# Optimization experiments

Measured on AMD Instinct MI355X. Metric: run time of the kernel, lower is better.

## Reference

```python
import jax, jax.numpy as jnp
import numpy as np

EPS = 1e-5


def _linear(x, w, b):
    # torch Linear: y = x @ w.T + b, w shape [out, in]
    return x @ w.T + b


def _batchnorm(x, gamma, beta):
    # training-mode BatchNorm1d: per-feature batch stats, biased variance
    m = jnp.mean(x, axis=0)
    v = jnp.var(x, axis=0)
    return (x - m) * jax.lax.rsqrt(v + EPS) * gamma + beta


def _noise_like(key, x):
    # mimics: mean = x.mean().item(); std = x.std().item() * U(1,2);
    # noise ~ N(mean, std) of x.shape, detached.
    ku, kn = jax.random.split(key)
    m = jax.lax.stop_gradient(jnp.mean(x))
    s = jax.lax.stop_gradient(jnp.std(x, ddof=1))
    u = jax.random.uniform(ku, (), dtype=x.dtype, minval=1.0, maxval=2.0)
    return m + s * u * jax.random.normal(kn, x.shape, dtype=x.dtype)


def setup_inputs() -> dict:
    key = jax.random.key(0)
    ks = jax.random.split(key, 12)
    B = 65536
    x = jax.random.normal(ks[0], (B, 784), dtype=jnp.float32)

    def lin_init(kw, kb, fan_in, fan_out):
        bound = 1.0 / np.sqrt(fan_in)
        w = jax.random.uniform(kw, (fan_out, fan_in), minval=-bound, maxval=bound, dtype=jnp.float32)
        b = jax.random.uniform(kb, (fan_out,), minval=-bound, maxval=bound, dtype=jnp.float32)
        return w, b

    w1, b1 = lin_init(ks[1], ks[2], 784, 48)
    w2, b2 = lin_init(ks[3], ks[4], 48, 24)
    w3, b3 = lin_init(ks[5], ks[6], 24, 10)
    return {
        "x": x,
        "w1": w1, "b1": b1,
        "gamma1": jnp.ones((48,), jnp.float32), "beta1": jnp.zeros((48,), jnp.float32),
        "w2": w2, "b2": b2,
        "gamma2": jnp.ones((24,), jnp.float32), "beta2": jnp.zeros((24,), jnp.float32),
        "w3": w3, "b3": b3,
    }


def reference(x, w1, b1, gamma1, beta1, w2, b2, gamma2, beta2, w3, b3):
    k1 = jax.random.key(1234)
    k2 = jax.random.key(5678)
    h = _batchnorm(_linear(x, w1, b1), gamma1, beta1)
    h = h + _noise_like(k1, h)
    h = jax.nn.relu(h)
    h = _batchnorm(_linear(h, w2, b2), gamma2, beta2)
    h = h + _noise_like(k2, h)
    h = jax.nn.relu(h)
    return _linear(h, w3, b3)
```

## Files before the change

### kernel.cpp

```cpp
#include <hip/hip_runtime.h>
#include <cstdint>
#include <cstring>


constexpr int MROWS = 65536;
constexpr int KDIM  = 784;
constexpr int KPAD  = 800;
constexpr int F1 = 48, F2 = 24, F3 = 10;

using frag_ab = __attribute__((ext_vector_type(8))) short;
using frag_cd = __attribute__((ext_vector_type(4))) float;

union UB { uint4 u; frag_ab f; };

__device__ __forceinline__ uint32_t rotl32(uint32_t v, int r) {
  return (v << r) | (v >> (32 - r));
}

__device__ __forceinline__ uint32_t tf_mix(uint32_t k0, uint32_t k1, uint32_t ctr) {
  uint32_t ks2 = k0 ^ k1 ^ 0x1BD11BDAu;
  uint32_t x0 = k0;
  uint32_t x1 = ctr + k1;
#define TFR(r) { x0 += x1; x1 = rotl32(x1, r); x1 ^= x0; }
  TFR(13) TFR(15) TFR(26) TFR(6)
  x0 += k1;  x1 += ks2 + 1u;
  TFR(17) TFR(29) TFR(16) TFR(24)
  x0 += ks2; x1 += k0 + 2u;
  TFR(13) TFR(15) TFR(26) TFR(6)
  x0 += k0;  x1 += k1 + 3u;
  TFR(17) TFR(29) TFR(16) TFR(24)
  x0 += k1;  x1 += ks2 + 4u;
  TFR(13) TFR(15) TFR(26) TFR(6)
  x0 += ks2; x1 += k0 + 5u;
#undef TFR
  return x0 ^ x1;
}

__device__ __forceinline__ float erfinv_f32(float x) {
  float t = fmaxf(1.0f - x * x, 1.0e-30f);
  float w = -__logf(t);
  float p;
  if (w < 5.0f) {
    w = w - 2.5f;
    p = 2.81022636e-08f;
    p = fmaf(p, w, 3.43273939e-07f);
    p = fmaf(p, w, -3.5233877e-06f);
    p = fmaf(p, w, -4.39150654e-06f);
    p = fmaf(p, w, 0.00021858087f);
    p = fmaf(p, w, -0.00125372503f);
    p = fmaf(p, w, -0.00417768164f);
    p = fmaf(p, w, 0.246640727f);
    p = fmaf(p, w, 1.50140941f);
  } else {
    w = sqrtf(w) - 3.0f;
    p = -0.000200214257f;
    p = fmaf(p, w, 0.000100950558f);
    p = fmaf(p, w, 0.00134934322f);
    p = fmaf(p, w, -0.00367342844f);
    p = fmaf(p, w, 0.00573950773f);
    p = fmaf(p, w, -0.0076224613f);
    p = fmaf(p, w, 0.00943887047f);
    p = fmaf(p, w, 1.00167406f);
    p = fmaf(p, w, 2.83297682f);
  }
  return p * x;
}

__device__ __forceinline__ float noise_normal(uint32_t k0, uint32_t k1, uint32_t ctr) {
  uint32_t bits = tf_mix(k0, k1, ctr);
  float f = __uint_as_float((bits >> 9) | 0x3f800000u) - 1.0f;
  const float lo = -0.99999994f;
  float u = fmaxf(lo, f * 2.0f + lo);
  return 1.41421356f * erfinv_f32(u);
}

__device__ __forceinline__ uint32_t pkbf(float a, float b) {
  uint32_t ua = __float_as_uint(a); ua += 0x7fffu + ((ua >> 16) & 1u);
  uint32_t ub = __float_as_uint(b); ub += 0x7fffu + ((ub >> 16) & 1u);
  return (ua >> 16) | (ub & 0xffff0000u);
}

__device__ __forceinline__ uint32_t cvtpk(float a, float b) {
  uint32_t r;
  asm("v_cvt_pk_bf16_f32 %0, %1, %2" : "=v"(r) : "v"(a), "v"(b));
  return r;
}

__global__ void k_prep(const float* __restrict__ w1, ushort* __restrict__ wb1,
                       float* __restrict__ st) {
  int i = blockIdx.x * 256 + threadIdx.x;
  if (i < 2048) st[i] = 0.f;
  if (i >= F1 * KPAD) return;
  int n = i / KPAD, k = i - n * KPAD;
  float v = (k < KDIM) ? w1[n * KDIM + k] : 0.f;
  uint32_t u = __float_as_uint(v);
  u += 0x7fffu + ((u >> 16) & 1u);
  wb1[i] = (ushort)(u >> 16);
}

__global__ __launch_bounds__(256, 4) void k_gemm1(
    const float* __restrict__ x, const ushort* __restrict__ wb1,
    const float* __restrict__ b1, float* __restrict__ h1,
    float* __restrict__ fsum, float* __restrict__ fssq) {
  __shared__ float reds[4][48], redq[4][48];

  const int t = threadIdx.x;
  const int w = t >> 6;
  const int l = t & 63;
  const int lane16 = l & 15;
  const int quad = l >> 4;
  const int rowbase = blockIdx.x * 64;
  const int myrow = rowbase + w * 16 + lane16;

  frag_cd acc[3];
#pragma unroll
  for (int ct = 0; ct < 3; ++ct)
#pragma unroll
    for (int r = 0; r < 4; ++r) acc[ct][r] = 0.f;

  const float* ap = x + (size_t)myrow * KDIM + quad * 8;
  const ushort* bp0 = wb1 + (size_t)(0 * 16 + lane16) * KPAD + quad * 8;
  const ushort* bp1 = wb1 + (size_t)(1 * 16 + lane16) * KPAD + quad * 8;
  const ushort* bp2 = wb1 + (size_t)(2 * 16 + lane16) * KPAD + quad * 8;

  float4 ca0 = *(const float4*)(ap);
  float4 ca1 = *(const float4*)(ap + 4);
  uint4 cb0 = *(const uint4*)(bp0);
  uint4 cb1 = *(const uint4*)(bp1);
  uint4 cb2 = *(const uint4*)(bp2);

  for (int s = 0; s < 25; ++s) {
    float4 na0 = make_float4(0.f, 0.f, 0.f, 0.f);
    float4 na1 = na0;
    uint4 nb0 = make_uint4(0, 0, 0, 0), nb1 = nb0, nb2 = nb0;
    if (s < 24) {
      const int ko = (s + 1) * 32;
      if (ko + quad * 8 + 8 <= KDIM) {
        na0 = *(const float4*)(ap + ko);
        na1 = *(const float4*)(ap + ko + 4);
      }
      nb0 = *(const uint4*)(bp0 + ko);
      nb1 = *(const uint4*)(bp1 + ko);
      nb2 = *(const uint4*)(bp2 + ko);
    }
    UB a;
    a.u.x = cvtpk(ca0.x, ca0.y);
    a.u.y = cvtpk(ca0.z, ca0.w);
    a.u.z = cvtpk(ca1.x, ca1.y);
    a.u.w = cvtpk(ca1.z, ca1.w);
    UB b;
    b.u = cb0; acc[0] = __builtin_amdgcn_mfma_f32_16x16x32_bf16(a.f, b.f, acc[0], 0, 0, 0);
    b.u = cb1; acc[1] = __builtin_amdgcn_mfma_f32_16x16x32_bf16(a.f, b.f, acc[1], 0, 0, 0);
    b.u = cb2; acc[2] = __builtin_amdgcn_mfma_f32_16x16x32_bf16(a.f, b.f, acc[2], 0, 0, 0);
    ca0 = na0; ca1 = na1; cb0 = nb0; cb1 = nb1; cb2 = nb2;
  }

  float bias[3];
#pragma unroll
  for (int ct = 0; ct < 3; ++ct) bias[ct] = b1[ct * 16 + lane16];
  float psum[3] = {0.f, 0.f, 0.f}, pssq[3] = {0.f, 0.f, 0.f};
#pragma unroll
  for (int r = 0; r < 4; ++r) {
    const int grow = rowbase + w * 16 + quad * 4 + r;
#pragma unroll
    for (int ct = 0; ct < 3; ++ct) {
      float v = acc[ct][r] + bias[ct];
      h1[(size_t)grow * F1 + ct * 16 + lane16] = v;
      psum[ct] += v;
      pssq[ct] += v * v;
    }
  }
#pragma unroll
  for (int ct = 0; ct < 3; ++ct) {
    psum[ct] += __shfl_xor(psum[ct], 16, 64);
    psum[ct] += __shfl_xor(psum[ct], 32, 64);
    pssq[ct] += __shfl_xor(pssq[ct], 16, 64);
    pssq[ct] += __shfl_xor(pssq[ct], 32, 64);
  }
  if (quad == 0) {
#pragma unroll
    for (int ct = 0; ct < 3; ++ct) {
      reds[w][ct * 16 + lane16] = psum[ct];
      redq[w][ct * 16 + lane16] = pssq[ct];
    }
  }
  __syncthreads();
  if (t < F1) {
    float s = reds[0][t] + reds[1][t] + reds[2][t] + reds[3][t];
    float q = redq[0][t] + redq[1][t] + redq[2][t] + redq[3][t];
    const int rep = blockIdx.x & 7;
    atomicAdd(&fsum[rep * 48 + t], s);
    atomicAdd(&fssq[rep * 48 + t], q);
  }
}

__global__ __launch_bounds__(256) void k_layer2(
    const float* __restrict__ h1, const float* __restrict__ w2,
    const float* __restrict__ b2, const float* __restrict__ gamma1,
    const float* __restrict__ beta1, const float* __restrict__ fsum,
    const float* __restrict__ fssq, float u1,
    float* __restrict__ h2, float* __restrict__ fsum2, float* __restrict__ fssq2,
    uint32_t kna, uint32_t knb) {
  __shared__ float a1s[64][49];
  __shared__ float w2s[48][25];
  __shared__ float h2s[64][25];
  __shared__ float bnp[4][48];
  __shared__ float scal[2];

  const int t = threadIdx.x;
  const int rowbase = blockIdx.x * 64;

  float cm = 0.f, cs = 0.f;
  if (t < F1) {
    float s0 = 0.f, q0 = 0.f;
#pragma unroll
    for (int rp = 0; rp < 8; ++rp) { s0 += fsum[rp * 48 + t]; q0 += fssq[rp * 48 + t]; }
    float m = s0 * (1.f / 65536.f);
    float v = q0 * (1.f / 65536.f) - m * m;
    float r = rsqrtf(v + 1e-5f);
    float g = gamma1[t], b = beta1[t];
    bnp[0][t] = m; bnp[1][t] = r; bnp[2][t] = g; bnp[3][t] = b;
    cm = b;
    cs = g * g * r * r * v + b * b;
  }
  if (t < 64) {
#pragma unroll
    for (int off = 32; off > 0; off >>= 1) {
      cm += __shfl_down(cm, off, 64);
      cs += __shfl_down(cs, off, 64);
    }
    if (t == 0) {
      float m = cm / (float)F1;
      float SS = 65536.f * cs;
      float Ntot = 65536.f * (float)F1;
      float s2 = (SS - Ntot * m * m) / (Ntot - 1.f);
      scal[0] = m;
      scal[1] = sqrtf(s2) * u1;
    }
  }
  for (int e = t; e < F2 * 48; e += 256) {
    int c = e / 48, k = e - c * 48;
    w2s[k][c] = w2[e];
  }
  __syncthreads();
  const float m1 = scal[0], su1 = scal[1];

  const int rr = t >> 2;
  const int cc0 = (t & 3) * 12;
  const int grow = rowbase + rr;
  const float* hrow = h1 + (size_t)grow * F1 + cc0;
#pragma unroll
  for (int jj = 0; jj < 12; jj += 4) {
    float4 hv = *(const float4*)(hrow + jj);
    float vv[4] = {hv.x, hv.y, hv.z, hv.w};
#pragma unroll
    for (int q = 0; q < 4; ++q) {
      int c = cc0 + jj + q;
      float bn = (vv[q] - bnp[0][c]) * bnp[1][c] * bnp[2][c] + bnp[3][c];
      uint32_t ctr = (uint32_t)grow * 48u + (uint32_t)c;
      float nz = noise_normal(kna, knb, ctr);
      float val = bn + fmaf(su1, nz, m1);
      a1s[rr][c] = fmaxf(val, 0.f);
    }
  }
  __syncthreads();

  const int rr2 = t & 63;
  const int c0 = (t >> 6) * 6;
  float acc[6] = {0.f, 0.f, 0.f, 0.f, 0.f, 0.f};
#pragma unroll
  for (int k = 0; k < 48; ++k) {
    float a = a1s[rr2][k];
#pragma unroll
    for (int j = 0; j < 6; ++j)
      acc[j] = fmaf(a, w2s[k][c0 + j], acc[j]);
  }
#pragma unroll
  for (int j = 0; j < 6; ++j)
    h2s[rr2][c0 + j] = acc[j] + b2[c0 + j];
  __syncthreads();

  for (int e = t; e < 64 * F2; e += 256) {
    int r2 = e / 24, c2 = e - r2 * 24;
    h2[(size_t)rowbase * F2 + e] = h2s[r2][c2];
  }
  if (t < F2) {
    float s = 0.f, q = 0.f;
    for (int r2 = 0; r2 < 64; ++r2) {
      float v = h2s[r2][t];
      s += v; q += v * v;
    }
    const int rep = blockIdx.x & 7;
    atomicAdd(&fsum2[rep * 24 + t], s);
    atomicAdd(&fssq2[rep * 24 + t], q);
  }
}

__global__ __launch_bounds__(256) void k_layer3(
    const float* __restrict__ h2, const float* __restrict__ w3,
    const float* __restrict__ b3, const float* __restrict__ gamma2,
    const float* __restrict__ beta2, const float* __restrict__ fsum2,
    const float* __restrict__ fssq2, float u2,
    float* __restrict__ out, uint32_t kna, uint32_t knb) {
  __shared__ float a2s[64][25];
  __shared__ float w3s[24][10];
  __shared__ float bnp[4][24];
  __shared__ float scal[2];

  const int t = threadIdx.x;
  const int rowbase = blockIdx.x * 64;

  float cm = 0.f, cs = 0.f;
  if (t < F2) {
    float s0 = 0.f, q0 = 0.f;
#pragma unroll
    for (int rp = 0; rp < 8; ++rp) { s0 += fsum2[rp * 24 + t]; q0 += fssq2[rp * 24 + t]; }
    float m = s0 * (1.f / 65536.f);
    float v = q0 * (1.f / 65536.f) - m * m;
    float r = rsqrtf(v + 1e-5f);
    float g = gamma2[t], b = beta2[t];
    bnp[0][t] = m; bnp[1][t] = r; bnp[2][t] = g; bnp[3][t] = b;
    cm = b;
    cs = g * g * r * r * v + b * b;
  }
  if (t < 64) {
#pragma unroll
    for (int off = 32; off > 0; off >>= 1) {
      cm += __shfl_down(cm, off, 64);
      cs += __shfl_down(cs, off, 64);
    }
    if (t == 0) {
      float m = cm / (float)F2;
      float SS = 65536.f * cs;
      float Ntot = 65536.f * (float)F2;
      float s2 = (SS - Ntot * m * m) / (Ntot - 1.f);
      scal[0] = m;
      scal[1] = sqrtf(s2) * u2;
    }
  }
  if (t < F3 * F2) {
    int c = t / 24, k = t - c * 24;
    w3s[k][c] = w3[t];
  }
  __syncthreads();
  const float m2 = scal[0], su2 = scal[1];

  for (int e = t; e < 64 * F2; e += 256) {
    int r = e / 24, c = e - r * 24;
    float v = h2[(size_t)rowbase * F2 + e];
    float bn = (v - bnp[0][c]) * bnp[1][c] * bnp[2][c] + bnp[3][c];
    uint32_t ctr = (uint32_t)(rowbase * F2 + e);
    float nz = noise_normal(kna, knb, ctr);
    float val = bn + fmaf(su2, nz, m2);
    a2s[r][c] = fmaxf(val, 0.f);
  }
  __syncthreads();

  if (t < 128) {
    const int rr = t & 63;
    const int c0 = (t >> 6) * 5;
    float acc[5] = {0.f, 0.f, 0.f, 0.f, 0.f};
#pragma unroll
    for (int k = 0; k < 24; ++k) {
      float a = a2s[rr][k];
#pragma unroll
      for (int j = 0; j < 5; ++j)
        acc[j] = fmaf(a, w3s[k][c0 + j], acc[j]);
    }
    size_t ob = (size_t)(rowbase + rr) * F3 + c0;
#pragma unroll
    for (int j = 0; j < 5; ++j) out[ob + j] = acc[j] + b3[c0 + j];
  }
}

static void host_tf(uint32_t k0, uint32_t k1, uint32_t c0, uint32_t c1,
                    uint32_t& o0, uint32_t& o1) {
  uint32_t ks2 = k0 ^ k1 ^ 0x1BD11BDAu;
  uint32_t x0 = c0 + k0, x1 = c1 + k1;
  auto R = [&](int r) { x0 += x1; x1 = (x1 << r) | (x1 >> (32 - r)); x1 ^= x0; };
  R(13); R(15); R(26); R(6);  x0 += k1;  x1 += ks2 + 1u;
  R(17); R(29); R(16); R(24); x0 += ks2; x1 += k0 + 2u;
  R(13); R(15); R(26); R(6);  x0 += k0;  x1 += k1 + 3u;
  R(17); R(29); R(16); R(24); x0 += k1;  x1 += ks2 + 4u;
  R(13); R(15); R(26); R(6);  x0 += ks2; x1 += k0 + 5u;
  o0 = x0; o1 = x1;
}

static float host_uniform12(uint32_t seed) {
  uint32_t ka, kb, t0, t1;
  host_tf(0u, seed, 0u, 0u, ka, kb);
  host_tf(ka, kb, 0u, 0u, t0, t1);
  uint32_t bits = t0 ^ t1;
  uint32_t fb = (bits >> 9) | 0x3f800000u;
  float f;
  std::memcpy(&f, &fb, 4);
  return f;
}

extern "C" void kernel_launch(void* const* d_in, const int* in_sizes, int n_in,
                              void* d_out, int out_size, void* d_ws, size_t ws_size,
                              hipStream_t stream) {
  (void)in_sizes; (void)n_in; (void)out_size; (void)ws_size;
  const float* x      = (const float*)d_in[0];
  const float* w1     = (const float*)d_in[1];
  const float* b1     = (const float*)d_in[2];
  const float* gamma1 = (const float*)d_in[3];
  const float* beta1  = (const float*)d_in[4];
  const float* w2     = (const float*)d_in[5];
  const float* b2     = (const float*)d_in[6];
  const float* gamma2 = (const float*)d_in[7];
  const float* beta2  = (const float*)d_in[8];
  const float* w3     = (const float*)d_in[9];
  const float* b3     = (const float*)d_in[10];
  float* out = (float*)d_out;

  float* h1 = (float*)d_ws;
  float* h2 = h1 + (size_t)MROWS * F1;
  float* st = h2 + (size_t)MROWS * F2;
  ushort* wb1 = (ushort*)(st + 2048);

  uint32_t kn1a, kn1b, kn2a, kn2b;
  host_tf(0u, 1234u, 0u, 1u, kn1a, kn1b);
  host_tf(0u, 5678u, 0u, 1u, kn2a, kn2b);
  float u1 = host_uniform12(1234u);
  float u2 = host_uniform12(5678u);

  k_prep<<<(F1 * KPAD + 255) / 256, 256, 0, stream>>>(w1, wb1, st);
  k_gemm1<<<MROWS / 64, 256, 0, stream>>>(x, wb1, b1, h1, st + 0, st + 384);
  k_layer2<<<MROWS / 64, 256, 0, stream>>>(h1, w2, b2, gamma1, beta1,
                                           st + 0, st + 384, u1,
                                           h2, st + 768, st + 960, kn1a, kn1b);
  k_layer3<<<MROWS / 64, 256, 0, stream>>>(h2, w3, b3, gamma2, beta2,
                                           st + 768, st + 960, u2,
                                           out, kn2a, kn2b);
}
```

Baseline: 78.01 us.

## Fuse all layers into one cooperative kernel with grid syncs and on-chip activations

Replaces the four separate kernels with a single cooperative kernel of 256 blocks x 512 threads. Each block owns 256 rows and keeps h1, h2 and the activations in LDS, using grid.sync for the batch-norm statistics barriers. This removes the global round trips of h1 and h2 and three launch boundaries. In exchange, only 256 blocks run (about one per CU), so the GEMM1 phase has less occupancy to hide the load latency of streaming x. The large LDS footprint and the grid-wide barriers add their own costs.

Result: slower. 269.2 us (+245.1%).

```diff
diff --git a/kernel.cpp b/kernel.cpp
--- a/kernel.cpp
+++ b/kernel.cpp
@@ -1,12 +1,18 @@
 #include <hip/hip_runtime.h>
+#include <hip/hip_cooperative_groups.h>
 #include <cstdint>
 #include <cstring>
+
+namespace cg = cooperative_groups;
 
 
 constexpr int MROWS = 65536;
 constexpr int KDIM  = 784;
 constexpr int KPAD  = 800;
 constexpr int F1 = 48, F2 = 24, F3 = 10;
+constexpr int NBLK = 256;
+constexpr int NTHR = 512;
+constexpr int RPB  = 256;
 
 using frag_ab = __attribute__((ext_vector_type(8))) short;
 using frag_cd = __attribute__((ext_vector_type(4))) float;
@@ -74,303 +80,334 @@
   return 1.41421356f * erfinv_f32(u);
 }
 
-__device__ __forceinline__ uint32_t pkbf(float a, float b) {
-  uint32_t ua = __float_as_uint(a); ua += 0x7fffu + ((ua >> 16) & 1u);
-  uint32_t ub = __float_as_uint(b); ub += 0x7fffu + ((ub >> 16) & 1u);
-  return (ua >> 16) | (ub & 0xffff0000u);
-}
-
 __device__ __forceinline__ uint32_t cvtpk(float a, float b) {
   uint32_t r;
   asm("v_cvt_pk_bf16_f32 %0, %1, %2" : "=v"(r) : "v"(a), "v"(b));
   return r;
 }
 
-__global__ void k_prep(const float* __restrict__ w1, ushort* __restrict__ wb1,
-                       float* __restrict__ st) {
-  int i = blockIdx.x * 256 + threadIdx.x;
-  if (i < 2048) st[i] = 0.f;
-  if (i >= F1 * KPAD) return;
-  int n = i / KPAD, k = i - n * KPAD;
-  float v = (k < KDIM) ? w1[n * KDIM + k] : 0.f;
-  uint32_t u = __float_as_uint(v);
-  u += 0x7fffu + ((u >> 16) & 1u);
-  wb1[i] = (ushort)(u >> 16);
-}
-
-__global__ __launch_bounds__(256, 4) void k_gemm1(
-    const float* __restrict__ x, const ushort* __restrict__ wb1,
-    const float* __restrict__ b1, float* __restrict__ h1,
-    float* __restrict__ fsum, float* __restrict__ fssq) {
-  __shared__ float reds[4][48], redq[4][48];
+__device__ __forceinline__ float ald(const float* p) {
+  return __hip_atomic_load(p, __ATOMIC_RELAXED, __HIP_MEMORY_SCOPE_AGENT);
+}
+__device__ __forceinline__ void ast(float* p, float v) {
+  __hip_atomic_store(p, v, __ATOMIC_RELAXED, __HIP_MEMORY_SCOPE_AGENT);
+}
+
+__global__ __launch_bounds__(NTHR, 2) void k_fused(
+    const float* __restrict__ x, const float* __restrict__ w1,
+    const float* __restrict__ b1, const float* __restrict__ gamma1,
+    const float* __restrict__ beta1, const float* __restrict__ w2,
+    const float* __restrict__ b2, const float* __restrict__ gamma2,
+    const float* __restrict__ beta2, const float* __restrict__ w3,
+    const float* __restrict__ b3, float* __restrict__ out,
+    ushort* __restrict__ wb1, float* __restrict__ st,
+    float u1, float u2, uint32_t kn1a, uint32_t kn1b,
+    uint32_t kn2a, uint32_t kn2b) {
+  __shared__ float h1s[RPB][49];
+  __shared__ float h2s[RPB][25];
+  __shared__ float a2s[RPB][25];
+  __shared__ float w2s[48][25];
+  __shared__ float w3s[24][10];
+  __shared__ float reds[8][48], redq[8][48];
+  __shared__ float bnp[4][48];
+  __shared__ float outs[RPB * F3];
+  __shared__ float scal[2];
 
   const int t = threadIdx.x;
-  const int w = t >> 6;
-  const int l = t & 63;
-  const int lane16 = l & 15;
-  const int quad = l >> 4;
-  const int rowbase = blockIdx.x * 64;
-  const int myrow = rowbase + w * 16 + lane16;
-
-  frag_cd acc[3];
-#pragma unroll
-  for (int ct = 0; ct < 3; ++ct)
-#pragma unroll
-    for (int r = 0; r < 4; ++r) acc[ct][r] = 0.f;
-
-  const float* ap = x + (size_t)myrow * KDIM + quad * 8;
-  const ushort* bp0 = wb1 + (size_t)(0 * 16 + lane16) * KPAD + quad * 8;
-  const ushort* bp1 = wb1 + (size_t)(1 * 16 + lane16) * KPAD + quad * 8;
-  const ushort* bp2 = wb1 + (size_t)(2 * 16 + lane16) * KPAD + quad * 8;
-
-  float4 ca0 = *(const float4*)(ap);
-  float4 ca1 = *(const float4*)(ap + 4);
-  uint4 cb0 = *(const uint4*)(bp0);
-  uint4 cb1 = *(const uint4*)(bp1);
-  uint4 cb2 = *(const uint4*)(bp2);
-
-  for (int s = 0; s < 25; ++s) {
-    float4 na0 = make_float4(0.f, 0.f, 0.f, 0.f);
-    float4 na1 = na0;
-    uint4 nb0 = make_uint4(0, 0, 0, 0), nb1 = nb0, nb2 = nb0;
-    if (s < 24) {
-      const int ko = (s + 1) * 32;
-      if (ko + quad * 8 + 8 <= KDIM) {
-        na0 = *(const float4*)(ap + ko);
-        na1 = *(const float4*)(ap + ko + 4);
-      }
-      nb0 = *(const uint4*)(bp0 + ko);
-      nb1 = *(const uint4*)(bp1 + ko);
-      nb2 = *(const uint4*)(bp2 + ko);
-    }
-    UB a;
-    a.u.x = cvtpk(ca0.x, ca0.y);
-    a.u.y = cvtpk(ca0.z, ca0.w);
-    a.u.z = cvtpk(ca1.x, ca1.y);
-    a.u.w = cvtpk(ca1.z, ca1.w);
-    UB b;
-    b.u = cb0; acc[0] = __builtin_amdgcn_mfma_f32_16x16x32_bf16(a.f, b.f, acc[0], 0, 0, 0);
-    b.u = cb1; acc[1] = __builtin_amdgcn_mfma_f32_16x16x32_bf16(a.f, b.f, acc[1], 0, 0, 0);
-    b.u = cb2; acc[2] = __builtin_amdgcn_mfma_f32_16x16x32_bf16(a.f, b.f, acc[2], 0, 0, 0);
-    ca0 = na0; ca1 = na1; cb0 = nb0; cb1 = nb1; cb2 = nb2;
-  }
-
-  float bias[3];
-#pragma unroll
-  for (int ct = 0; ct < 3; ++ct) bias[ct] = b1[ct * 16 + lane16];
-  float psum[3] = {0.f, 0.f, 0.f}, pssq[3] = {0.f, 0.f, 0.f};
-#pragma unroll
-  for (int r = 0; r < 4; ++r) {
-    const int grow = rowbase + w * 16 + quad * 4 + r;
+  const int rowbase = blockIdx.x * RPB;
+  cg::grid_group grid = cg::this_grid();
+
+  {
+    int gid = blockIdx.x * NTHR + t;
+    if (gid < 2048) ast(&st[gid], 0.f);
+    if (gid < F1 * KPAD) {
+      int n = gid / KPAD, k = gid - n * KPAD;
+      float v = (k < KDIM) ? w1[n * KDIM + k] : 0.f;
+      uint32_t u = __float_as_uint(v);
+      u += 0x7fffu + ((u >> 16) & 1u);
+      wb1[gid] = (ushort)(u >> 16);
+    }
+  }
+  __threadfence();
+  grid.sync();
+
+  {
+    const int w = t >> 6, l = t & 63;
+    const int lane16 = l & 15, quad = l >> 4;
+    frag_cd acc[2][3];
+#pragma unroll
+    for (int g = 0; g < 2; ++g)
+#pragma unroll
+      for (int ct = 0; ct < 3; ++ct)
+#pragma unroll
+        for (int r = 0; r < 4; ++r) acc[g][ct][r] = 0.f;
+
+    const float* ap0 = x + (size_t)(rowbase + w * 32 + lane16) * KDIM + quad * 8;
+    const float* ap1 = ap0 + (size_t)16 * KDIM;
+    const ushort* bp0 = wb1 + (size_t)lane16 * KPAD + quad * 8;
+    const ushort* bp1 = bp0 + 16 * KPAD;
+    const ushort* bp2 = bp0 + 32 * KPAD;
+
+    float4 a00 = *(const float4*)(ap0);
+    float4 a01 = *(const float4*)(ap0 + 4);
+    float4 a10 = *(const float4*)(ap1);
+    float4 a11 = *(const float4*)(ap1 + 4);
+    uint4 cb0 = *(const uint4*)(bp0);
+    uint4 cb1 = *(const uint4*)(bp1);
+    uint4 cb2 = *(const uint4*)(bp2);
+
+    for (int s = 0; s < 25; ++s) {
+      float4 n00 = make_float4(0.f, 0.f, 0.f, 0.f), n01 = n00, n10 = n00, n11 = n00;
+      uint4 nb0 = make_uint4(0, 0, 0, 0), nb1 = nb0, nb2 = nb0;
+      if (s < 24) {
+        const int ko = (s + 1) * 32;
+        if (ko + quad * 8 + 8 <= KDIM) {
+          n00 = *(const float4*)(ap0 + ko);
+          n01 = *(const float4*)(ap0 + ko + 4);
+          n10 = *(const float4*)(ap1 + ko);
+          n11 = *(const float4*)(ap1 + ko + 4);
+        }
+        nb0 = *(const uint4*)(bp0 + ko);
+        nb1 = *(const uint4*)(bp1 + ko);
+        nb2 = *(const uint4*)(bp2 + ko);
+      }
+      UB A0, A1;
+      A0.u.x = cvtpk(a00.x, a00.y);
+      A0.u.y = cvtpk(a00.z, a00.w);
+      A0.u.z = cvtpk(a01.x, a01.y);
+      A0.u.w = cvtpk(a01.z, a01.w);
+      A1.u.x = cvtpk(a10.x, a10.y);
+      A1.u.y = cvtpk(a10.z, a10.w);
+      A1.u.z = cvtpk(a11.x, a11.y);
+      A1.u.w = cvtpk(a11.z, a11.w);
+      UB B;
+      B.u = cb0;
+      acc[0][0] = __builtin_amdgcn_mfma_f32_16x16x32_bf16(A0.f, B.f, acc[0][0], 0, 0, 0);
+      acc[1][0] = __builtin_amdgcn_mfma_f32_16x16x32_bf16(A1.f, B.f, acc[1][0], 0, 0, 0);
+      B.u = cb1;
+      acc[0][1] = __builtin_amdgcn_mfma_f32_16x16x32_bf16(A0.f, B.f, acc[0][1], 0, 0, 0);
+      acc[1][1] = __builtin_amdgcn_mfma_f32_16x16x32_bf16(A1.f, B.f, acc[1][1], 0, 0, 0);
+      B.u = cb2;
+      acc[0][2] = __builtin_amdgcn_mfma_f32_16x16x32_bf16(A0.f, B.f, acc[0][2], 0, 0, 0);
+      acc[1][2] = __builtin_amdgcn_mfma_f32_16x16x32_bf16(A1.f, B.f, acc[1][2], 0, 0, 0);
+      a00 = n00; a01 = n01; a10 = n10; a11 = n11;
+      cb0 = nb0; cb1 = nb1; cb2 = nb2;
+    }
+
+    float bias[3];
+#pragma unroll
+    for (int ct = 0; ct < 3; ++ct) bias[ct] = b1[ct * 16 + lane16];
+    float psum[3] = {0.f, 0.f, 0.f}, pssq[3] = {0.f, 0.f, 0.f};
+#pragma unroll
+    for (int g = 0; g < 2; ++g)
+#pragma unroll
+      for (int r = 0; r < 4; ++r) {
+        const int lrow = w * 32 + g * 16 + quad * 4 + r;
+#pragma unroll
+        for (int ct = 0; ct < 3; ++ct) {
+          float v = acc[g][ct][r] + bias[ct];
+          h1s[lrow][ct * 16 + lane16] = v;
+          psum[ct] += v;
+          pssq[ct] += v * v;
+        }
+      }
 #pragma unroll
     for (int ct = 0; ct < 3; ++ct) {
-      float v = acc[ct][r] + bias[ct];
-      h1[(size_t)grow * F1 + ct * 16 + lane16] = v;
-      psum[ct] += v;
-      pssq[ct] += v * v;
-    }
-  }
-#pragma unroll
-  for (int ct = 0; ct < 3; ++ct) {
-    psum[ct] += __shfl_xor(psum[ct], 16, 64);
-    psum[ct] += __shfl_xor(psum[ct], 32, 64);
-    pssq[ct] += __shfl_xor(pssq[ct], 16, 64);
-    pssq[ct] += __shfl_xor(pssq[ct], 32, 64);
-  }
-  if (quad == 0) {
-#pragma unroll
-    for (int ct = 0; ct < 3; ++ct) {
-      reds[w][ct * 16 + lane16] = psum[ct];
-      redq[w][ct * 16 + lane16] = pssq[ct];
+      psum[ct] += __shfl_xor(psum[ct], 16, 64);
+      psum[ct] += __shfl_xor(psum[ct], 32, 64);
+      pssq[ct] += __shfl_xor(pssq[ct], 16, 64);
+      pssq[ct] += __shfl_xor(pssq[ct], 32, 64);
+    }
+    if (quad == 0) {
+#pragma unroll
+      for (int ct = 0; ct < 3; ++ct) {
+        reds[w][ct * 16 + lane16] = psum[ct];
+        redq[w][ct * 16 + lane16] = pssq[ct];
+      }
     }
   }
   __syncthreads();
   if (t < F1) {
-    float s = reds[0][t] + reds[1][t] + reds[2][t] + reds[3][t];
-    float q = redq[0][t] + redq[1][t] + redq[2][t] + redq[3][t];
+    float s = 0.f, q = 0.f;
+#pragma unroll
+    for (int w = 0; w < 8; ++w) { s += reds[w][t]; q += redq[w][t]; }
     const int rep = blockIdx.x & 7;
-    atomicAdd(&fsum[rep * 48 + t], s);
-    atomicAdd(&fssq[rep * 48 + t], q);
-  }
-}
-
-__global__ __launch_bounds__(256) void k_layer2(
-    const float* __restrict__ h1, const float* __restrict__ w2,
-    const float* __restrict__ b2, const float* __restrict__ gamma1,
-    const float* __restrict__ beta1, const float* __restrict__ fsum,
-    const float* __restrict__ fssq, float u1,
-    float* __restrict__ h2, float* __restrict__ fsum2, float* __restrict__ fssq2,
-    uint32_t kna, uint32_t knb) {
-  __shared__ float a1s[64][49];
-  __shared__ float w2s[48][25];
-  __shared__ float h2s[64][25];
-  __shared__ float bnp[4][48];
-  __shared__ float scal[2];
-
-  const int t = threadIdx.x;
-  const int rowbase = blockIdx.x * 64;
-
-  float cm = 0.f, cs = 0.f;
-  if (t < F1) {
-    float s0 = 0.f, q0 = 0.f;
-#pragma unroll
-    for (int rp = 0; rp < 8; ++rp) { s0 += fsum[rp * 48 + t]; q0 += fssq[rp * 48 + t]; }
-    float m = s0 * (1.f / 65536.f);
-    float v = q0 * (1.f / 65536.f) - m * m;
-    float r = rsqrtf(v + 1e-5f);
-    float g = gamma1[t], b = beta1[t];
-    bnp[0][t] = m; bnp[1][t] = r; bnp[2][t] = g; bnp[3][t] = b;
-    cm = b;
-    cs = g * g * r * r * v + b * b;
-  }
-  if (t < 64) {
-#pragma unroll
-    for (int off = 32; off > 0; off >>= 1) {
-      cm += __shfl_down(cm, off, 64);
-      cs += __shfl_down(cs, off, 64);
-    }
-    if (t == 0) {
-      float m = cm / (float)F1;
-      float SS = 65536.f * cs;
-      float Ntot = 65536.f * (float)F1;
-      float s2 = (SS - Ntot * m * m) / (Ntot - 1.f);
-      scal[0] = m;
-      scal[1] = sqrtf(s2) * u1;
-    }
-  }
-  for (int e = t; e < F2 * 48; e += 256) {
-    int c = e / 48, k = e - c * 48;
-    w2s[k][c] = w2[e];
-  }
-  __syncthreads();
-  const float m1 = scal[0], su1 = scal[1];
-
-  const int rr = t >> 2;
-  const int cc0 = (t & 3) * 12;
-  const int grow = rowbase + rr;
-  const float* hrow = h1 + (size_t)grow * F1 + cc0;
-#pragma unroll
-  for (int jj = 0; jj < 12; jj += 4) {
-    float4 hv = *(const float4*)(hrow + jj);
-    float vv[4] = {hv.x, hv.y, hv.z, hv.w};
-#pragma unroll
-    for (int q = 0; q < 4; ++q) {
-      int c = cc0 + jj + q;
-      float bn = (vv[q] - bnp[0][c]) * bnp[1][c] * bnp[2][c] + bnp[3][c];
-      uint32_t ctr = (uint32_t)grow * 48u + (uint32_t)c;
-      float nz = noise_normal(kna, knb, ctr);
-      float val = bn + fmaf(su1, nz, m1);
-      a1s[rr][c] = fmaxf(val, 0.f);
-    }
-  }
-  __syncthreads();
-
-  const int rr2 = t & 63;
-  const int c0 = (t >> 6) * 6;
-  float acc[6] = {0.f, 0.f, 0.f, 0.f, 0.f, 0.f};
-#pragma unroll
-  for (int k = 0; k < 48; ++k) {
-    float a = a1s[rr2][k];
-#pragma unroll
-    for (int j = 0; j < 6; ++j)
-      acc[j] = fmaf(a, w2s[k][c0 + j], acc[j]);
-  }
-#pragma unroll
-  for (int j = 0; j < 6; ++j)
-    h2s[rr2][c0 + j] = acc[j] + b2[c0 + j];
-  __syncthreads();
-
-  for (int e = t; e < 64 * F2; e += 256) {
-    int r2 = e / 24, c2 = e - r2 * 24;
-    h2[(size_t)rowbase * F2 + e] = h2s[r2][c2];
-  }
+    atomicAdd(&st[rep * 48 + t], s);
+    atomicAdd(&st[384 + rep * 48 + t], q);
+  }
+  __threadfence();
+  grid.sync();
+
+  {
+    float cm = 0.f, cs = 0.f;
+    if (t < F1) {
+      float s0 = 0.f, q0 = 0.f;
+#pragma unroll
+      for (int rp = 0; rp < 8; ++rp) {
+        s0 += ald(&st[rp * 48 + t]);
+        q0 += ald(&st[384 + rp * 48 + t]);
+      }
+      float m = s0 * (1.f / 65536.f);
+      float v = q0 * (1.f / 65536.f) - m * m;
+      float r = rsqrtf(v + 1e-5f);
+      float g = gamma1[t], b = beta1[t];
+      bnp[0][t] = m; bnp[1][t] = r; bnp[2][t] = g; bnp[3][t] = b;
+      cm = b;
+      cs = g * g * r * r * v + b * b;
+    }
+    if (t < 64) {
+#pragma unroll
+      for (int off = 32; off > 0; off >>= 1) {
+        cm += __shfl_down(cm, off, 64);
+        cs += __shfl_down(cs, off, 64);
+      }
+      if (t == 0) {
+        float m = cm / (float)F1;
+        float SS = 65536.f * cs;
+        float Ntot = 65536.f * (float)F1;
+        float s2 = (SS - Ntot * m * m) / (Ntot - 1.f);
+        scal[0] = m;
+        scal[1] = sqrtf(s2) * u1;
+      }
+    }
+    for (int e = t; e < F2 * 48; e += NTHR) {
+      int c = e / 48, k = e - c * 48;
+      w2s[k][c] = w2[e];
+    }
+  }
+  __syncthreads();
+  {
+    const float m1 = scal[0], su1 = scal[1];
+#pragma unroll
+    for (int p = 0; p < 2; ++p) {
+      const int rr = p * 128 + (t >> 2);
+      const int cc0 = (t & 3) * 12;
+      const int grow = rowbase + rr;
+      const uint32_t cbase = (uint32_t)grow * 48u + (uint32_t)cc0;
+#pragma unroll
+      for (int j = 0; j < 12; ++j) {
+        int c = cc0 + j;
+        float v = h1s[rr][c];
+        float bn = (v - bnp[0][c]) * bnp[1][c] * bnp[2][c] + bnp[3][c];
+        float nz = noise_normal(kn1a, kn1b, cbase + (uint32_t)j);
+        float val = bn + fmaf(su1, nz, m1);
+        h1s[rr][c] = fmaxf(val, 0.f);
+      }
+    }
+  }
+  __syncthreads();
+  {
+    const int c0 = (t >> 7) * 6;
+    float bb[6];
+#pragma unroll
+    for (int j = 0; j < 6; ++j) bb[j] = b2[c0 + j];
+#pragma unroll
+    for (int p = 0; p < 2; ++p) {
+      const int row = p * 128 + (t & 127);
+      float acc2[6] = {0.f, 0.f, 0.f, 0.f, 0.f, 0.f};
+#pragma unroll
+      for (int k = 0; k < 48; ++k) {
+        float a = h1s[row][k];
+#pragma unroll
+        for (int j = 0; j < 6; ++j) acc2[j] = fmaf(a, w2s[k][c0 + j], acc2[j]);
+      }
+#pragma unroll
+      for (int j = 0; j < 6; ++j) h2s[row][c0 + j] = acc2[j] + bb[j];
+    }
+  }
+  __syncthreads();
+  if (t < 192) {
+    const int c = t % 24, ch = t / 24;
+    float s = 0.f, q = 0.f;
+#pragma unroll 8
+    for (int r = ch * 32; r < ch * 32 + 32; ++r) {
+      float v = h2s[r][c];
+      s += v; q += v * v;
+    }
+    reds[ch][c] = s; redq[ch][c] = q;
+  }
+  __syncthreads();
   if (t < F2) {
     float s = 0.f, q = 0.f;
-    for (int r2 = 0; r2 < 64; ++r2) {
-      float v = h2s[r2][t];
-      s += v; q += v * v;
-    }
+#pragma unroll
+    for (int ch = 0; ch < 8; ++ch) { s += reds[ch][t]; q += redq[ch][t]; }
     const int rep = blockIdx.x & 7;
-    atomicAdd(&fsum2[rep * 24 + t], s);
-    atomicAdd(&fssq2[rep * 24 + t], q);
-  }
-}
-
-__global__ __launch_bounds__(256) void k_layer3(
-    const float* __restrict__ h2, const float* __restrict__ w3,
-    const float* __restrict__ b3, const float* __restrict__ gamma2,
-    const float* __restrict__ beta2, const float* __restrict__ fsum2,
-    const float* __restrict__ fssq2, float u2,
-    float* __restrict__ out, uint32_t kna, uint32_t knb) {
-  __shared__ float a2s[64][25];
-  __shared__ float w3s[24][10];
-  __shared__ float bnp[4][24];
-  __shared__ float scal[2];
-
-  const int t = threadIdx.x;
-  const int rowbase = blockIdx.x * 64;
-
-  float cm = 0.f, cs = 0.f;
-  if (t < F2) {
-    float s0 = 0.f, q0 = 0.f;
-#pragma unroll
-    for (int rp = 0; rp < 8; ++rp) { s0 += fsum2[rp * 24 + t]; q0 += fssq2[rp * 24 + t]; }
-    float m = s0 * (1.f / 65536.f);
-    float v = q0 * (1.f / 65536.f) - m * m;
-    float r = rsqrtf(v + 1e-5f);
-    float g = gamma2[t], b = beta2[t];
-    bnp[0][t] = m; bnp[1][t] = r; bnp[2][t] = g; bnp[3][t] = b;
-    cm = b;
-    cs = g * g * r * r * v + b * b;
-  }
-  if (t < 64) {
-#pragma unroll
-    for (int off = 32; off > 0; off >>= 1) {
-      cm += __shfl_down(cm, off, 64);
-      cs += __shfl_down(cs, off, 64);
-    }
-    if (t == 0) {
-      float m = cm / (float)F2;
-      float SS = 65536.f * cs;
-      float Ntot = 65536.f * (float)F2;
-      float s2 = (SS - Ntot * m * m) / (Ntot - 1.f);
-      scal[0] = m;
-      scal[1] = sqrtf(s2) * u2;
-    }
-  }
-  if (t < F3 * F2) {
-    int c = t / 24, k = t - c * 24;
-    w3s[k][c] = w3[t];
-  }
-  __syncthreads();
-  const float m2 = scal[0], su2 = scal[1];
-
-  for (int e = t; e < 64 * F2; e += 256) {
-    int r = e / 24, c = e - r * 24;
-    float v = h2[(size_t)rowbase * F2 + e];
-    float bn = (v - bnp[0][c]) * bnp[1][c] * bnp[2][c] + bnp[3][c];
-    uint32_t ctr = (uint32_t)(rowbase * F2 + e);
-    float nz = noise_normal(kna, knb, ctr);
-    float val = bn + fmaf(su2, nz, m2);
-    a2s[r][c] = fmaxf(val, 0.f);
-  }
-  __syncthreads();
-
-  if (t < 128) {
-    const int rr = t & 63;
-    const int c0 = (t >> 6) * 5;
-    float acc[5] = {0.f, 0.f, 0.f, 0.f, 0.f};
+    atomicAdd(&st[768 + rep * 24 + t], s);
+    atomicAdd(&st[960 + rep * 24 + t], q);
+  }
+  __threadfence();
+  grid.sync();
+
+  {
+    float cm = 0.f, cs = 0.f;
+    if (t < F2) {
+      float s0 = 0.f, q0 = 0.f;
+#pragma unroll
+      for (int rp = 0; rp < 8; ++rp) {
+        s0 += ald(&st[768 + rp * 24 + t]);
+        q0 += ald(&st[960 + rp * 24 + t]);
+      }
+      float m = s0 * (1.f / 65536.f);
+      float v = q0 * (1.f / 65536.f) - m * m;
+      float r = rsqrtf(v + 1e-5f);
+      float g = gamma2[t], b = beta2[t];
+      bnp[0][t] = m; bnp[1][t] = r; bnp[2][t] = g; bnp[3][t] = b;
+      cm = b;
+      cs = g * g * r * r * v + b * b;
+    }
+    if (t < 64) {
+#pragma unroll
+      for (int off = 32; off > 0; off >>= 1) {
+        cm += __shfl_down(cm, off, 64);
+        cs += __shfl_down(cs, off, 64);
+      }
+      if (t == 0) {
+        float m = cm / (float)F2;
+        float SS = 65536.f * cs;
+        float Ntot = 65536.f * (float)F2;
+        float s2 = (SS - Ntot * m * m) / (Ntot - 1.f);
+        scal[0] = m;
+        scal[1] = sqrtf(s2) * u2;
+      }
+    }
+    if (t < F3 * F2) {
+      int c = t / 24, k = t - c * 24;
+      w3s[k][c] = w3[t];
+    }
+  }
+  __syncthreads();
+  {
+    const float m2 = scal[0], su2 = scal[1];
+    for (int e = t; e < RPB * F2; e += NTHR) {
+      int r = e / 24, c = e - r * 24;
+      float v = h2s[r][c];
+      float bn = (v - bnp[0][c]) * bnp[1][c] * bnp[2][c] + bnp[3][c];
+      uint32_t ctr = (uint32_t)rowbase * 24u + (uint32_t)e;
+      float nz = noise_normal(kn2a, kn2b, ctr);
+      float val = bn + fmaf(su2, nz, m2);
+      a2s[r][c] = fmaxf(val, 0.f);
+    }
+  }
+  __syncthreads();
+  {
+    const int rr = t & 255;
+    const int c0 = (t >> 8) * 5;
+    float bb3[5];
+#pragma unroll
+    for (int j = 0; j < 5; ++j) bb3[j] = b3[c0 + j];
+    float acc3[5] = {0.f, 0.f, 0.f, 0.f, 0.f};
 #pragma unroll
     for (int k = 0; k < 24; ++k) {
       float a = a2s[rr][k];
 #pragma unroll
-      for (int j = 0; j < 5; ++j)
-        acc[j] = fmaf(a, w3s[k][c0 + j], acc[j]);
-    }
-    size_t ob = (size_t)(rowbase + rr) * F3 + c0;
-#pragma unroll
-    for (int j = 0; j < 5; ++j) out[ob + j] = acc[j] + b3[c0 + j];
-  }
+      for (int j = 0; j < 5; ++j) acc3[j] = fmaf(a, w3s[k][c0 + j], acc3[j]);
+    }
+#pragma unroll
+    for (int j = 0; j < 5; ++j) outs[rr * F3 + c0 + j] = acc3[j] + bb3[j];
+  }
+  __syncthreads();
+  for (int e = t; e < RPB * F3; e += NTHR)
+    out[(size_t)rowbase * F3 + e] = outs[e];
 }
 
 static void host_tf(uint32_t k0, uint32_t k1, uint32_t c0, uint32_t c1,
@@ -414,9 +451,7 @@
   const float* b3     = (const float*)d_in[10];
   float* out = (float*)d_out;
 
-  float* h1 = (float*)d_ws;
-  float* h2 = h1 + (size_t)MROWS * F1;
-  float* st = h2 + (size_t)MROWS * F2;
+  float* st = (float*)d_ws;
   ushort* wb1 = (ushort*)(st + 2048);
 
   uint32_t kn1a, kn1b, kn2a, kn2b;
@@ -425,12 +460,12 @@
   float u1 = host_uniform12(1234u);
   float u2 = host_uniform12(5678u);
 
-  k_prep<<<(F1 * KPAD + 255) / 256, 256, 0, stream>>>(w1, wb1, st);
-  k_gemm1<<<MROWS / 64, 256, 0, stream>>>(x, wb1, b1, h1, st + 0, st + 384);
-  k_layer2<<<MROWS / 64, 256, 0, stream>>>(h1, w2, b2, gamma1, beta1,
-                                           st + 0, st + 384, u1,
-                                           h2, st + 768, st + 960, kn1a, kn1b);
-  k_layer3<<<MROWS / 64, 256, 0, stream>>>(h2, w3, b3, gamma2, beta2,
-                                           st + 768, st + 960, u2,
-                                           out, kn2a, kn2b);
-}
+  void* args[] = {
+    (void*)&x, (void*)&w1, (void*)&b1, (void*)&gamma1, (void*)&beta1,
+    (void*)&w2, (void*)&b2, (void*)&gamma2, (void*)&beta2,
+    (void*)&w3, (void*)&b3, (void*)&out, (void*)&wb1, (void*)&st,
+    (void*)&u1, (void*)&u2,
+    (void*)&kn1a, (void*)&kn1b, (void*)&kn2a, (void*)&kn2b};
+  hipLaunchCooperativeKernel(reinterpret_cast<void*>(k_fused),
+                             dim3(NBLK), dim3(NTHR), args, 0, stream);
+}
```

## Fuse layer2 and layer3 into one kernel with a grid-wide atomic barrier

Applied to the files above, without the earlier changes.

Merges the layer-2 and layer-3 kernels into a single k_tail kernel. A global atomic counter acts as a grid barrier, so every block waits until all blocks have added their layer-2 BN statistics before it normalizes. This keeps h2 in shared memory, which removes the h2 global write and read-back and one kernel launch. The barrier relies on all 1024 blocks being co-resident (launch_bounds 256,4), and a spin-wait stalls the whole grid on the slowest block.

After: 250.2 us. 221% more time.

```diff
diff --git a/kernel.cpp b/kernel.cpp
--- a/kernel.cpp
+++ b/kernel.cpp
@@ -7,6 +7,7 @@
 constexpr int KDIM  = 784;
 constexpr int KPAD  = 800;
 constexpr int F1 = 48, F2 = 24, F3 = 10;
+constexpr int NBLK = 1024;
 
 using frag_ab = __attribute__((ext_vector_type(8))) short;
 using frag_cd = __attribute__((ext_vector_type(4))) float;
@@ -74,22 +75,20 @@
   return 1.41421356f * erfinv_f32(u);
 }
 
-__device__ __forceinline__ uint32_t pkbf(float a, float b) {
-  uint32_t ua = __float_as_uint(a); ua += 0x7fffu + ((ua >> 16) & 1u);
-  uint32_t ub = __float_as_uint(b); ub += 0x7fffu + ((ub >> 16) & 1u);
-  return (ua >> 16) | (ub & 0xffff0000u);
-}
-
 __device__ __forceinline__ uint32_t cvtpk(float a, float b) {
   uint32_t r;
   asm("v_cvt_pk_bf16_f32 %0, %1, %2" : "=v"(r) : "v"(a), "v"(b));
   return r;
 }
 
+__device__ __forceinline__ float ald(const float* p) {
+  return __hip_atomic_load(p, __ATOMIC_RELAXED, __HIP_MEMORY_SCOPE_AGENT);
+}
+
 __global__ void k_prep(const float* __restrict__ w1, ushort* __restrict__ wb1,
                        float* __restrict__ st) {
   int i = blockIdx.x * 256 + threadIdx.x;
-  if (i < 2048) st[i] = 0.f;
+  if (i < 2064) st[i] = 0.f;
   if (i >= F1 * KPAD) return;
   int n = i / KPAD, k = i - n * KPAD;
   float v = (k < KDIM) ? w1[n * KDIM + k] : 0.f;
@@ -194,96 +193,102 @@
   }
 }
 
-__global__ __launch_bounds__(256) void k_layer2(
+__global__ __launch_bounds__(256, 4) void k_tail(
     const float* __restrict__ h1, const float* __restrict__ w2,
     const float* __restrict__ b2, const float* __restrict__ gamma1,
-    const float* __restrict__ beta1, const float* __restrict__ fsum,
-    const float* __restrict__ fssq, float u1,
-    float* __restrict__ h2, float* __restrict__ fsum2, float* __restrict__ fssq2,
-    uint32_t kna, uint32_t knb) {
+    const float* __restrict__ beta1, const float* __restrict__ gamma2,
+    const float* __restrict__ beta2, const float* __restrict__ w3,
+    const float* __restrict__ b3, const float* __restrict__ fsum,
+    const float* __restrict__ fssq, float* __restrict__ fsum2,
+    float* __restrict__ fssq2, uint32_t* __restrict__ fl,
+    float u1, float u2, uint32_t kn1a, uint32_t kn1b,
+    uint32_t kn2a, uint32_t kn2b, float* __restrict__ out) {
   __shared__ float a1s[64][49];
   __shared__ float w2s[48][25];
   __shared__ float h2s[64][25];
   __shared__ float bnp[4][48];
+  __shared__ float w3s[24][10];
   __shared__ float scal[2];
 
   const int t = threadIdx.x;
   const int rowbase = blockIdx.x * 64;
 
-  float cm = 0.f, cs = 0.f;
-  if (t < F1) {
-    float s0 = 0.f, q0 = 0.f;
-#pragma unroll
-    for (int rp = 0; rp < 8; ++rp) { s0 += fsum[rp * 48 + t]; q0 += fssq[rp * 48 + t]; }
-    float m = s0 * (1.f / 65536.f);
-    float v = q0 * (1.f / 65536.f) - m * m;
-    float r = rsqrtf(v + 1e-5f);
-    float g = gamma1[t], b = beta1[t];
-    bnp[0][t] = m; bnp[1][t] = r; bnp[2][t] = g; bnp[3][t] = b;
-    cm = b;
-    cs = g * g * r * r * v + b * b;
-  }
-  if (t < 64) {
-#pragma unroll
-    for (int off = 32; off > 0; off >>= 1) {
-      cm += __shfl_down(cm, off, 64);
-      cs += __shfl_down(cs, off, 64);
-    }
-    if (t == 0) {
-      float m = cm / (float)F1;
-      float SS = 65536.f * cs;
-      float Ntot = 65536.f * (float)F1;
-      float s2 = (SS - Ntot * m * m) / (Ntot - 1.f);
-      scal[0] = m;
-      scal[1] = sqrtf(s2) * u1;
-    }
-  }
-  for (int e = t; e < F2 * 48; e += 256) {
-    int c = e / 48, k = e - c * 48;
-    w2s[k][c] = w2[e];
-  }
-  __syncthreads();
-  const float m1 = scal[0], su1 = scal[1];
-
-  const int rr = t >> 2;
-  const int cc0 = (t & 3) * 12;
-  const int grow = rowbase + rr;
-  const float* hrow = h1 + (size_t)grow * F1 + cc0;
-#pragma unroll
-  for (int jj = 0; jj < 12; jj += 4) {
-    float4 hv = *(const float4*)(hrow + jj);
-    float vv[4] = {hv.x, hv.y, hv.z, hv.w};
-#pragma unroll
-    for (int q = 0; q < 4; ++q) {
-      int c = cc0 + jj + q;
-      float bn = (vv[q] - bnp[0][c]) * bnp[1][c] * bnp[2][c] + bnp[3][c];
-      uint32_t ctr = (uint32_t)grow * 48u + (uint32_t)c;
-      float nz = noise_normal(kna, knb, ctr);
-      float val = bn + fmaf(su1, nz, m1);
-      a1s[rr][c] = fmaxf(val, 0.f);
-    }
-  }
-  __syncthreads();
-
-  const int rr2 = t & 63;
-  const int c0 = (t >> 6) * 6;
-  float acc[6] = {0.f, 0.f, 0.f, 0.f, 0.f, 0.f};
-#pragma unroll
-  for (int k = 0; k < 48; ++k) {
-    float a = a1s[rr2][k];
+  {
+    float cm = 0.f, cs = 0.f;
+    if (t < F1) {
+      float s0 = 0.f, q0 = 0.f;
+#pragma unroll
+      for (int rp = 0; rp < 8; ++rp) { s0 += fsum[rp * 48 + t]; q0 += fssq[rp * 48 + t]; }
+      float m = s0 * (1.f / 65536.f);
+      float v = q0 * (1.f / 65536.f) - m * m;
+      float r = rsqrtf(v + 1e-5f);
+      float g = gamma1[t], b = beta1[t];
+      bnp[0][t] = m; bnp[1][t] = r; bnp[2][t] = g; bnp[3][t] = b;
+      cm = b;
+      cs = g * g * r * r * v + b * b;
+    }
+    if (t < 64) {
+#pragma unroll
+      for (int off = 32; off > 0; off >>= 1) {
+        cm += __shfl_down(cm, off, 64);
+        cs += __shfl_down(cs, off, 64);
+      }
+      if (t == 0) {
+        float m = cm / (float)F1;
+        float SS = 65536.f * cs;
+        float Ntot = 65536.f * (float)F1;
+        float s2 = (SS - Ntot * m * m) / (Ntot - 1.f);
+        scal[0] = m;
+        scal[1] = sqrtf(s2) * u1;
+      }
+    }
+    for (int e = t; e < F2 * 48; e += 256) {
+      int c = e / 48, k = e - c * 48;
+      w2s[k][c] = w2[e];
+    }
+  }
+  __syncthreads();
+
+  {
+    const float m1 = scal[0], su1 = scal[1];
+    const int rr = t >> 2;
+    const int cc0 = (t & 3) * 12;
+    const int grow = rowbase + rr;
+    const float* hrow = h1 + (size_t)grow * F1 + cc0;
+    const uint32_t cbase = (uint32_t)grow * 48u + (uint32_t)cc0;
+#pragma unroll
+    for (int jj = 0; jj < 12; jj += 4) {
+      float4 hv = *(const float4*)(hrow + jj);
+      float vv[4] = {hv.x, hv.y, hv.z, hv.w};
+#pragma unroll
+      for (int q = 0; q < 4; ++q) {
+        int c = cc0 + jj + q;
+        float bn = (vv[q] - bnp[0][c]) * bnp[1][c] * bnp[2][c] + bnp[3][c];
+        float nz = noise_normal(kn1a, kn1b, cbase + (uint32_t)(jj + q));
+        float val = bn + fmaf(su1, nz, m1);
+        a1s[rr][c] = fmaxf(val, 0.f);
+      }
+    }
+  }
+  __syncthreads();
+
+  {
+    const int rr2 = t & 63;
+    const int c0 = (t >> 6) * 6;
+    float acc2[6] = {0.f, 0.f, 0.f, 0.f, 0.f, 0.f};
+#pragma unroll
+    for (int k = 0; k < 48; ++k) {
+      float a = a1s[rr2][k];
+#pragma unroll
+      for (int j = 0; j < 6; ++j)
+        acc2[j] = fmaf(a, w2s[k][c0 + j], acc2[j]);
+    }
 #pragma unroll
     for (int j = 0; j < 6; ++j)
-      acc[j] = fmaf(a, w2s[k][c0 + j], acc[j]);
-  }
-#pragma unroll
-  for (int j = 0; j < 6; ++j)
-    h2s[rr2][c0 + j] = acc[j] + b2[c0 + j];
-  __syncthreads();
-
-  for (int e = t; e < 64 * F2; e += 256) {
-    int r2 = e / 24, c2 = e - r2 * 24;
-    h2[(size_t)rowbase * F2 + e] = h2s[r2][c2];
-  }
+      h2s[rr2][c0 + j] = acc2[j] + b2[c0 + j];
+  }
+  __syncthreads();
+
   if (t < F2) {
     float s = 0.f, q = 0.f;
     for (int r2 = 0; r2 < 64; ++r2) {
@@ -294,82 +299,87 @@
     atomicAdd(&fsum2[rep * 24 + t], s);
     atomicAdd(&fssq2[rep * 24 + t], q);
   }
-}
-
-__global__ __launch_bounds__(256) void k_layer3(
-    const float* __restrict__ h2, const float* __restrict__ w3,
-    const float* __restrict__ b3, const float* __restrict__ gamma2,
-    const float* __restrict__ beta2, const float* __restrict__ fsum2,
-    const float* __restrict__ fssq2, float u2,
-    float* __restrict__ out, uint32_t kna, uint32_t knb) {
-  __shared__ float a2s[64][25];
-  __shared__ float w3s[24][10];
-  __shared__ float bnp[4][24];
-  __shared__ float scal[2];
-
-  const int t = threadIdx.x;
-  const int rowbase = blockIdx.x * 64;
-
-  float cm = 0.f, cs = 0.f;
-  if (t < F2) {
-    float s0 = 0.f, q0 = 0.f;
-#pragma unroll
-    for (int rp = 0; rp < 8; ++rp) { s0 += fsum2[rp * 24 + t]; q0 += fssq2[rp * 24 + t]; }
-    float m = s0 * (1.f / 65536.f);
-    float v = q0 * (1.f / 65536.f) - m * m;
-    float r = rsqrtf(v + 1e-5f);
-    float g = gamma2[t], b = beta2[t];
-    bnp[0][t] = m; bnp[1][t] = r; bnp[2][t] = g; bnp[3][t] = b;
-    cm = b;
-    cs = g * g * r * r * v + b * b;
-  }
-  if (t < 64) {
-#pragma unroll
-    for (int off = 32; off > 0; off >>= 1) {
-      cm += __shfl_down(cm, off, 64);
-      cs += __shfl_down(cs, off, 64);
-    }
-    if (t == 0) {
-      float m = cm / (float)F2;
-      float SS = 65536.f * cs;
-      float Ntot = 65536.f * (float)F2;
-      float s2 = (SS - Ntot * m * m) / (Ntot - 1.f);
-      scal[0] = m;
-      scal[1] = sqrtf(s2) * u2;
-    }
-  }
+  __threadfence();
+  __syncthreads();
+
+  if (t == 0)
+    __hip_atomic_fetch_add(&fl[0], 1u, __ATOMIC_RELEASE, __HIP_MEMORY_SCOPE_AGENT);
   if (t < F3 * F2) {
     int c = t / 24, k = t - c * 24;
     w3s[k][c] = w3[t];
   }
-  __syncthreads();
-  const float m2 = scal[0], su2 = scal[1];
-
-  for (int e = t; e < 64 * F2; e += 256) {
-    int r = e / 24, c = e - r * 24;
-    float v = h2[(size_t)rowbase * F2 + e];
-    float bn = (v - bnp[0][c]) * bnp[1][c] * bnp[2][c] + bnp[3][c];
-    uint32_t ctr = (uint32_t)(rowbase * F2 + e);
-    float nz = noise_normal(kna, knb, ctr);
-    float val = bn + fmaf(su2, nz, m2);
-    a2s[r][c] = fmaxf(val, 0.f);
+  if (t == 0) {
+    while (__hip_atomic_load(&fl[0], __ATOMIC_ACQUIRE, __HIP_MEMORY_SCOPE_AGENT) < (uint32_t)NBLK)
+      __builtin_amdgcn_s_sleep(8);
+  }
+  __syncthreads();
+  __threadfence();
+
+  {
+    float cm = 0.f, cs = 0.f;
+    if (t < F2) {
+      float s0 = 0.f, q0 = 0.f;
+#pragma unroll
+      for (int rp = 0; rp < 8; ++rp) {
+        s0 += ald(&fsum2[rp * 24 + t]);
+        q0 += ald(&fssq2[rp * 24 + t]);
+      }
+      float m = s0 * (1.f / 65536.f);
+      float v = q0 * (1.f / 65536.f) - m * m;
+      float r = rsqrtf(v + 1e-5f);
+      float g = gamma2[t], b = beta2[t];
+      bnp[0][t] = m; bnp[1][t] = r; bnp[2][t] = g; bnp[3][t] = b;
+      cm = b;
+      cs = g * g * r * r * v + b * b;
+    }
+    if (t < 64) {
+#pragma unroll
+      for (int off = 32; off > 0; off >>= 1) {
+        cm += __shfl_down(cm, off, 64);
+        cs += __shfl_down(cs, off, 64);
+      }
+      if (t == 0) {
+        float m = cm / (float)F2;
+        float SS = 65536.f * cs;
+        float Ntot = 65536.f * (float)F2;
+        float s2 = (SS - Ntot * m * m) / (Ntot - 1.f);
+        scal[0] = m;
+        scal[1] = sqrtf(s2) * u2;
+      }
+    }
+  }
+  __syncthreads();
+
+  {
+    const float m2 = scal[0], su2 = scal[1];
+#pragma unroll
+    for (int i = 0; i < 6; ++i) {
+      int e = t + i * 256;
+      int r = e / 24, c = e - r * 24;
+      float v = h2s[r][c];
+      float bn = (v - bnp[0][c]) * bnp[1][c] * bnp[2][c] + bnp[3][c];
+      uint32_t ctr = (uint32_t)rowbase * 24u + (uint32_t)e;
+      float nz = noise_normal(kn2a, kn2b, ctr);
+      float val = bn + fmaf(su2, nz, m2);
+      a1s[r][c] = fmaxf(val, 0.f);
+    }
   }
   __syncthreads();
 
   if (t < 128) {
     const int rr = t & 63;
     const int c0 = (t >> 6) * 5;
-    float acc[5] = {0.f, 0.f, 0.f, 0.f, 0.f};
+    float acc3[5] = {0.f, 0.f, 0.f, 0.f, 0.f};
 #pragma unroll
     for (int k = 0; k < 24; ++k) {
-      float a = a2s[rr][k];
+      float a = a1s[rr][k];
 #pragma unroll
       for (int j = 0; j < 5; ++j)
-        acc[j] = fmaf(a, w3s[k][c0 + j], acc[j]);
+        acc3[j] = fmaf(a, w3s[k][c0 + j], acc3[j]);
     }
     size_t ob = (size_t)(rowbase + rr) * F3 + c0;
 #pragma unroll
-    for (int j = 0; j < 5; ++j) out[ob + j] = acc[j] + b3[c0 + j];
+    for (int j = 0; j < 5; ++j) out[ob + j] = acc3[j] + b3[c0 + j];
   }
 }
 
@@ -415,9 +425,9 @@
   float* out = (float*)d_out;
 
   float* h1 = (float*)d_ws;
-  float* h2 = h1 + (size_t)MROWS * F1;
-  float* st = h2 + (size_t)MROWS * F2;
-  ushort* wb1 = (ushort*)(st + 2048);
+  float* st = h1 + (size_t)MROWS * F1;
+  uint32_t* fli = (uint32_t*)(st + 2048);
+  ushort* wb1 = (ushort*)(st + 2064);
 
   uint32_t kn1a, kn1b, kn2a, kn2b;
   host_tf(0u, 1234u, 0u, 1u, kn1a, kn1b);
@@ -426,11 +436,8 @@
   float u2 = host_uniform12(5678u);
 
   k_prep<<<(F1 * KPAD + 255) / 256, 256, 0, stream>>>(w1, wb1, st);
-  k_gemm1<<<MROWS / 64, 256, 0, stream>>>(x, wb1, b1, h1, st + 0, st + 384);
-  k_layer2<<<MROWS / 64, 256, 0, stream>>>(h1, w2, b2, gamma1, beta1,
-                                           st + 0, st + 384, u1,
-                                           h2, st + 768, st + 960, kn1a, kn1b);
-  k_layer3<<<MROWS / 64, 256, 0, stream>>>(h2, w3, b3, gamma2, beta2,
-                                           st + 768, st + 960, u2,
-                                           out, kn2a, kn2b);
-}
+  k_gemm1<<<NBLK, 256, 0, stream>>>(x, wb1, b1, h1, st + 0, st + 384);
+  k_tail<<<NBLK, 256, 0, stream>>>(h1, w2, b2, gamma1, beta1, gamma2, beta2,
+                                   w3, b3, st + 0, st + 384, st + 768, st + 960,
+                                   fli, u1, u2, kn1a, kn1b, kn2a, kn2b, out);
+}
```
